# Performance work log

Hardware: AMD Instinct MI355X
Metric: run time of the kernel (lower is better)

Reference implementation:

```python
import jax, jax.numpy as jnp
import numpy as np

B, S, D = 2, 2048, 1024
H = 16
HD = D // H
SCALE = HD ** (-0.5)


def setup_inputs() -> dict:
    key = jax.random.key(0)
    k1, k2, k3, k4 = jax.random.split(key, 4)
    x = jax.random.normal(k1, (B, S, D), dtype=jnp.float32)
    # nn.Linear-style init scale to keep activations sane
    w_qkv = jax.random.normal(k2, (3 * D, D), dtype=jnp.float32) * (D ** -0.5)
    w_out = jax.random.normal(k3, (D, D), dtype=jnp.float32) * (D ** -0.5)
    b_out = jax.random.normal(k4, (D,), dtype=jnp.float32) * 0.01
    return {"x": x, "w_qkv": w_qkv, "w_out": w_out, "b_out": b_out}


def reference(x, w_qkv, w_out, b_out):
    b, s, d = x.shape
    # qkv projection (no bias): [b, s, 3d]
    qkv = jnp.einsum('bsd,ed->bse', x, w_qkv)
    # Rearrange 'b c (e h hd) -> e b h c hd'
    qkv = qkv.reshape(b, s, 3, H, HD).transpose(2, 0, 3, 1, 4)
    # NOTE: original splits as (v, q, k) in that order
    v, q, k = qkv[0], qkv[1], qkv[2]
    # scale applied after matmul, as in the original
    scores = jnp.einsum('bhqd,bhkd->bhqk', q, k) * SCALE
    attn = jax.nn.softmax(scores, axis=-1)
    o = jnp.einsum('bhqk,bhkd->bhqd', attn, v)
    # 'b h c hd -> b c (h hd)'
    o = o.transpose(0, 2, 1, 3).reshape(b, s, d)
    return jnp.einsum('bsd,ed->bse', o, w_out) + b_out
```

## Files before the change

kernel.cpp:

```cpp
#include <hip/hip_runtime.h>
#include <cstdint>
#include <cstddef>

#define BB 2
#define SS 2048
#define DD 1024
#define HH 16
#define HDIM 64

typedef short bf16x8 __attribute__((ext_vector_type(8)));
typedef short bf16x4 __attribute__((ext_vector_type(4)));
typedef float f32x4 __attribute__((ext_vector_type(4)));
typedef float f32x2 __attribute__((ext_vector_type(2)));

union U4S8 { uint4 u; bf16x8 s; };
union U2S4 { uint2 u; bf16x4 s; unsigned short h[4]; };

#if defined(__HIP_DEVICE_COMPILE__)
# if __has_builtin(__builtin_amdgcn_mfma_f32_16x16x16bf16_1k)
#  define MFMA_PV(a, b, c) __builtin_amdgcn_mfma_f32_16x16x16bf16_1k((a), (b), (c), 0, 0, 0)
# else
#  define MFMA_PV(a, b, c) __builtin_amdgcn_mfma_f32_16x16x16_bf16((a), (b), (c), 0, 0, 0)
# endif
# if __has_builtin(__builtin_amdgcn_exp2f)
#  define EXP2(x) __builtin_amdgcn_exp2f(x)
# else
#  define EXP2(x) exp2f(x)
# endif
#else
# define MFMA_PV(a, b, c) (c)
# define EXP2(x) exp2f(x)
#endif

__device__ __forceinline__ unsigned short f2bf(float f) {
    union { float f; unsigned int u; } c; c.f = f;
    unsigned int u = c.u;
    unsigned int r = (u + 0x7FFFu + ((u >> 16) & 1u)) >> 16;
    return (unsigned short)r;
}

__device__ __forceinline__ void async_cp16(const void* g, void* l) {
    __builtin_amdgcn_global_load_lds(
        (const __attribute__((address_space(1))) void*)g,
        (__attribute__((address_space(3))) void*)l, 16, 0, 0);
}

__global__ __launch_bounds__(256) void cvt_all(
    const float* __restrict__ x, const float* __restrict__ wq,
    const float* __restrict__ wo,
    unsigned short* __restrict__ xb, unsigned short* __restrict__ wqb,
    unsigned short* __restrict__ wob) {
    int i = blockIdx.x * 256 + threadIdx.x;
    const float* in; unsigned short* out; int j;
    if (i < 524288)       { in = x;  out = xb;  j = i; }
    else if (i < 917504)  { in = wq; out = wqb; j = i - 524288; }
    else                  { in = wo; out = wob; j = i - 917504; }
    float4 a = ((const float4*)in)[2 * j];
    float4 b = ((const float4*)in)[2 * j + 1];
    union { uint4 u; unsigned short h[8]; } o;
    o.h[0] = f2bf(a.x); o.h[1] = f2bf(a.y); o.h[2] = f2bf(a.z); o.h[3] = f2bf(a.w);
    o.h[4] = f2bf(b.x); o.h[5] = f2bf(b.y); o.h[6] = f2bf(b.z); o.h[7] = f2bf(b.w);
    ((uint4*)out)[j] = o.u;
}

__global__ __launch_bounds__(256) void gemm_qkv(
    const unsigned short* __restrict__ A,
    const unsigned short* __restrict__ Bw,
    unsigned short* __restrict__ qb, unsigned short* __restrict__ kb,
    unsigned short* __restrict__ vb) {
    const int K = 1024;
    __shared__ unsigned short smem[18432];
    int tid = threadIdx.x;
    int lane = tid & 63, wave = tid >> 6;
    int wm = (wave & 1) * 64, wn = (wave >> 1) * 64;
    int m0 = blockIdx.y * 128, n0 = blockIdx.x * 128;
    int lm = lane & 15, lq = lane >> 4;

    f32x4 acc[4][4] = {};

    int sdst = tid * 8;
    const unsigned short* gA = A  + (size_t)(m0 + (tid >> 2)) * K + (tid & 3) * 8;
    const unsigned short* gB = Bw + (size_t)(n0 + (tid >> 2)) * K + (tid & 3) * 8;

#define GSTAGE(k0, buf) do {                                          \
        async_cp16(gA + (k0),          smem + (buf) + sdst);          \
        async_cp16(gA + 64 * K + (k0), smem + (buf) + 2048 + sdst);   \
        async_cp16(gB + (k0),          smem + (buf) + 4096 + sdst);   \
        async_cp16(gB + 64 * K + (k0), smem + (buf) + 6144 + sdst);   \
    } while (0)

    GSTAGE(0, 0);
    for (int k0 = 0; k0 < K; k0 += 64) {
        #pragma unroll
        for (int hf = 0; hf < 2; hf++) {
            int base = hf ? 8192 : 0;
            int obuf = hf ? 0 : 8192;
            __syncthreads();
            int kn = k0 + 32 + hf * 32;
            if (kn < K) GSTAGE(kn, obuf);
            const unsigned short* As = smem + base;
            const unsigned short* Bs = smem + base + 4096;
            U4S8 af[4], bfx[4];
            #pragma unroll
            for (int i = 0; i < 4; i++) {
                af[i].u  = *(const uint4*)(As + (wm + i * 16 + lm) * 32 + lq * 8);
                bfx[i].u = *(const uint4*)(Bs + (wn + i * 16 + lm) * 32 + lq * 8);
            }
            #pragma unroll
            for (int mi = 0; mi < 4; mi++)
                #pragma unroll
                for (int ni = 0; ni < 4; ni++)
                    acc[mi][ni] = __builtin_amdgcn_mfma_f32_16x16x32_bf16(
                        af[mi].s, bfx[ni].s, acc[mi][ni], 0, 0, 0);
        }
    }
#undef GSTAGE
    __syncthreads();

    unsigned short* Lw = smem + wave * 4608;
    int b = m0 >> 11;
    int s_base = (m0 + wm) & 2047;
    if (n0 < 1024) {
        int h = (n0 + wn) >> 6;
        #pragma unroll
        for (int mi = 0; mi < 4; mi++)
            #pragma unroll
            for (int ni = 0; ni < 4; ni++)
                #pragma unroll
                for (int r = 0; r < 4; r++)
                    Lw[(ni * 16 + lm) * 72 + mi * 16 + lq * 4 + r] =
                        f2bf(acc[mi][ni][r]);
        __builtin_amdgcn_wave_barrier();
        unsigned short* vdst = vb + ((size_t)(b * HH + h) * HDIM) * SS + s_base;
        #pragma unroll
        for (int it = 0; it < 8; it++) {
            int hd = it * 8 + (lane >> 3);
            int so = (lane & 7) * 8;
            uint4 val = *(const uint4*)&Lw[hd * 72 + so];
            *(uint4*)(vdst + (size_t)hd * SS + so) = val;
        }
    } else {
        bool isq = n0 < 2048;
        unsigned short* dst = isq ? qb : kb;
        float scale = isq ? 0.18033688f : 1.0f;
        int h = ((n0 + wn) >> 6) & 15;
        #pragma unroll
        for (int mi = 0; mi < 4; mi++)
            #pragma unroll
            for (int ni = 0; ni < 4; ni++)
                #pragma unroll
                for (int r = 0; r < 4; r++)
                    Lw[(mi * 16 + lq * 4 + r) * 72 + ni * 16 + lm] =
                        f2bf(acc[mi][ni][r] * scale);
        __builtin_amdgcn_wave_barrier();
        unsigned short* qdst =
            dst + ((size_t)(b * HH + h) * SS + s_base) * HDIM;
        #pragma unroll
        for (int it = 0; it < 8; it++) {
            int srw = it * 8 + (lane >> 3);
            int so = (lane & 7) * 8;
            uint4 val = *(const uint4*)&Lw[srw * 72 + so];
            *(uint4*)(qdst + (size_t)srw * HDIM + so) = val;
        }
    }
}

__global__ __launch_bounds__(512) void attn(
    const unsigned short* __restrict__ qb,
    const unsigned short* __restrict__ kb,
    const unsigned short* __restrict__ vb,
    unsigned short* __restrict__ ob) {
    int bh = blockIdx.y;
    int q0 = blockIdx.x * 128;
    int tid = threadIdx.x, lane = tid & 63, wave = tid >> 6;
    int grp = wave >> 2;
    int w4  = wave & 3;
    int lm = lane & 15, lq = lane >> 4;

    __shared__ unsigned short smem[32768];
    float* smf = (float*)smem;

    const unsigned short* qg = qb + (size_t)bh * SS * HDIM;
    const unsigned short* kg = kb + (size_t)bh * SS * HDIM;
    const unsigned short* vg = vb + (size_t)bh * HDIM * SS;

    U4S8 qf[2][2];
    #pragma unroll
    for (int qt = 0; qt < 2; qt++)
        #pragma unroll
        for (int ks = 0; ks < 2; ks++)
            qf[qt][ks].u = *(const uint4*)(
                qg + (size_t)(q0 + w4 * 32 + qt * 16 + lm) * HDIM + ks * 32 + lq * 8);

    f32x4 oacc[4][2] = {};
    f32x2 lsum2[2] = {};

    int lm7 = lm & 7;
    int kidx = lm * 64 + 8 * (lq ^ lm7);
    int vidx[4];
    #pragma unroll
    for (int kc = 0; kc < 4; kc++)
        vidx[kc] = lm * 64 + 8 * (((kc << 1) | (lq >> 1)) ^ lm7) + (lq & 1) * 4;

    int srow = tid >> 3;
    int lch  = (tid & 7) ^ (srow & 7);
    int sdst = tid * 8;
    const unsigned short* kpA = kg + (size_t)srow * HDIM + lch * 8;
    const unsigned short* kpB = kpA + 64 * HDIM;
    const unsigned short* vpA = vg + (size_t)srow * SS + lch * 8;
    const unsigned short* vpB = vpA + 64;

    #define STAGE(pbase)                                                       \
        do {                                                                   \
            async_cp16(kpA, smem + (pbase) + sdst);                            \
            async_cp16(kpB, smem + (pbase) + 4096 + sdst);                     \
            async_cp16(vpA, smem + (pbase) + 8192 + sdst);                     \
            async_cp16(vpB, smem + (pbase) + 12288 + sdst);                    \
            kpA += 128 * HDIM; kpB += 128 * HDIM; vpA += 128; vpB += 128;      \
        } while (0)

    STAGE(0);

    for (int kt = 0; kt < SS / 128; kt += 2) {
        #pragma unroll
        for (int hf = 0; hf < 2; hf++) {
            int cbase = hf ? 16384 : 0;
            int obase = hf ? 0 : 16384;
            __syncthreads();
            STAGE(obase);

            int kbase = cbase + grp * 4096;
            int vbase = cbase + 8192 + grp * 4096;

            U2S4 pb[4][2];
            #pragma unroll
            for (int mi = 0; mi < 4; mi++) {
                U4S8 kf0, kf1;
                kf0.u = *(const uint4*)(smem + kbase + mi * 1024 + kidx);
                kf1.u = *(const uint4*)(smem + kbase + mi * 1024 + (kidx ^ 32));
                #pragma unroll
                for (int qt = 0; qt < 2; qt++) {
                    f32x4 sa = {};
                    sa = __builtin_amdgcn_mfma_f32_16x16x32_bf16(kf0.s, qf[qt][0].s, sa, 0, 0, 0);
                    sa = __builtin_amdgcn_mfma_f32_16x16x32_bf16(kf1.s, qf[qt][1].s, sa, 0, 0, 0);
                    float p0 = EXP2(sa[0]);
                    float p1 = EXP2(sa[1]);
                    float p2 = EXP2(sa[2]);
                    float p3 = EXP2(sa[3]);
                    f32x2 a01; a01[0] = p0; a01[1] = p1;
                    f32x2 a23; a23[0] = p2; a23[1] = p3;
                    lsum2[qt] += a01;
                    lsum2[qt] += a23;
                    unsigned int b0 = __float_as_uint(p0) + 0x8000u;
                    unsigned int b1 = __float_as_uint(p1) + 0x8000u;
                    unsigned int b2 = __float_as_uint(p2) + 0x8000u;
                    unsigned int b3 = __float_as_uint(p3) + 0x8000u;
                    pb[mi][qt].u.x = __builtin_amdgcn_perm(b1, b0, 0x07060302u);
                    pb[mi][qt].u.y = __builtin_amdgcn_perm(b3, b2, 0x07060302u);
                }
            }

            #pragma unroll
            for (int mi2 = 0; mi2 < 4; mi2++) {
                #pragma unroll
                for (int kc = 0; kc < 4; kc++) {
                    U2S4 vf;
                    vf.u = *(const uint2*)(smem + vbase + mi2 * 1024 + vidx[kc]);
                    oacc[mi2][0] = MFMA_PV(vf.s, pb[kc][0].s, oacc[mi2][0]);
                    oacc[mi2][1] = MFMA_PV(vf.s, pb[kc][1].s, oacc[mi2][1]);
                }
            }
        }
    }
    #undef STAGE

    float gsum[2];
    #pragma unroll
    for (int qt = 0; qt < 2; qt++) {
        float s = lsum2[qt][0] + lsum2[qt][1];
        s += __shfl_xor(s, 16);
        s += __shfl_xor(s, 32);
        gsum[qt] = s;
    }

    __syncthreads();

    if (grp == 1) {
        float* pub = smf + w4 * 2048;
        #pragma unroll
        for (int mi2 = 0; mi2 < 4; mi2++)
            #pragma unroll
            for (int qt = 0; qt < 2; qt++)
                #pragma unroll
                for (int r = 0; r < 4; r++)
                    pub[(mi2 * 8 + qt * 4 + r) * 64 + lane] = oacc[mi2][qt][r];
        if (lq == 0) {
            smf[8192 + w4 * 32 + lm]      = gsum[0];
            smf[8192 + w4 * 32 + 16 + lm] = gsum[1];
        }
    }
    __syncthreads();

    if (grp == 0) {
        float* pub = smf + w4 * 2048;
        #pragma unroll
        for (int mi2 = 0; mi2 < 4; mi2++)
            #pragma unroll
            for (int qt = 0; qt < 2; qt++)
                #pragma unroll
                for (int r = 0; r < 4; r++)
                    oacc[mi2][qt][r] += pub[(mi2 * 8 + qt * 4 + r) * 64 + lane];
        float inv[2];
        inv[0] = 1.f / (gsum[0] + smf[8192 + w4 * 32 + lm]);
        inv[1] = 1.f / (gsum[1] + smf[8192 + w4 * 32 + 16 + lm]);

        unsigned short* Ow = smem + 17024 + w4 * 2304;
        #pragma unroll
        for (int mi2 = 0; mi2 < 4; mi2++)
            #pragma unroll
            for (int qt = 0; qt < 2; qt++) {
                U2S4 t;
                #pragma unroll
                for (int r = 0; r < 4; r++)
                    t.h[r] = f2bf(oacc[mi2][qt][r] * inv[qt]);
                *(uint2*)&Ow[(qt * 16 + lm) * 72 + mi2 * 16 + lq * 4] = t.u;
            }
        __builtin_amdgcn_wave_barrier();
        int b = bh >> 4, h = bh & 15;
        #pragma unroll
        for (int it = 0; it < 4; it++) {
            int q  = it * 8 + (lane >> 3);
            int off = (lane & 7) * 8;
            uint4 val = *(const uint4*)&Ow[q * 72 + off];
            int srw = q0 + w4 * 32 + q;
            *(uint4*)(ob + (size_t)(b * SS + srw) * DD + h * 64 + off) = val;
        }
    }
}

__global__ __launch_bounds__(256) void gemm_out(
    const unsigned short* __restrict__ A,
    const unsigned short* __restrict__ Bw,
    const float* __restrict__ bias, float* __restrict__ out) {
    const int K = 1024;
    __shared__ unsigned short smem[12288];
    int tid = threadIdx.x;
    int lane = tid & 63, wave = tid >> 6;
    int wm = (wave & 1) * 64, wn = (wave >> 1) * 32;
    int m0 = blockIdx.y * 128, n0 = blockIdx.x * 64;
    int lm = lane & 15, lq = lane >> 4;

    f32x4 acc[4][2] = {};

    int sdst = tid * 8;
    const unsigned short* gA = A  + (size_t)(m0 + (tid >> 2)) * K + (tid & 3) * 8;
    const unsigned short* gB = Bw + (size_t)(n0 + (tid >> 2)) * K + (tid & 3) * 8;

#define OSTAGE(k0, buf) do {                                          \
        async_cp16(gA + (k0),          smem + (buf) + sdst);          \
        async_cp16(gA + 64 * K + (k0), smem + (buf) + 2048 + sdst);   \
        async_cp16(gB + (k0),          smem + (buf) + 4096 + sdst);   \
    } while (0)

    OSTAGE(0, 0);
    for (int k0 = 0; k0 < K; k0 += 64) {
        #pragma unroll
        for (int hf = 0; hf < 2; hf++) {
            int base = hf ? 6144 : 0;
            int obuf = hf ? 0 : 6144;
            __syncthreads();
            int kn = k0 + 32 + hf * 32;
            if (kn < K) OSTAGE(kn, obuf);
            const unsigned short* As = smem + base;
            const unsigned short* Bs = smem + base + 4096;
            U4S8 af[4], bfx[2];
            #pragma unroll
            for (int i = 0; i < 4; i++)
                af[i].u = *(const uint4*)(As + (wm + i * 16 + lm) * 32 + lq * 8);
            #pragma unroll
            for (int i = 0; i < 2; i++)
                bfx[i].u = *(const uint4*)(Bs + (wn + i * 16 + lm) * 32 + lq * 8);
            #pragma unroll
            for (int mi = 0; mi < 4; mi++)
                #pragma unroll
                for (int ni = 0; ni < 2; ni++)
                    acc[mi][ni] = __builtin_amdgcn_mfma_f32_16x16x32_bf16(
                        af[mi].s, bfx[ni].s, acc[mi][ni], 0, 0, 0);
        }
    }
#undef OSTAGE

    #pragma unroll
    for (int mi = 0; mi < 4; mi++) {
        int gr = m0 + wm + mi * 16 + lq * 4;
        #pragma unroll
        for (int ni = 0; ni < 2; ni++) {
            int gc = n0 + wn + ni * 16 + lm;
            float bv = bias[gc];
            #pragma unroll
            for (int r = 0; r < 4; r++)
                out[(size_t)(gr + r) * DD + gc] = acc[mi][ni][r] + bv;
        }
    }
}

extern "C" void kernel_launch(void* const* d_in, const int* in_sizes, int n_in,
                              void* d_out, int out_size, void* d_ws, size_t ws_size,
                              hipStream_t stream) {
    const float* x     = (const float*)d_in[0];
    const float* w_qkv = (const float*)d_in[1];
    const float* w_out = (const float*)d_in[2];
    const float* b_out = (const float*)d_in[3];
    float* out = (float*)d_out;

    unsigned short* ws = (unsigned short*)d_ws;
    const size_t NX = (size_t)BB * SS * DD;
    unsigned short* x_bf    = ws;
    unsigned short* wqkv_bf = x_bf + NX;
    unsigned short* wout_bf = wqkv_bf + 3145728;
    unsigned short* q_buf   = wout_bf + 1048576;
    unsigned short* k_buf   = q_buf + NX;
    unsigned short* v_buf   = k_buf + NX;
    unsigned short* o_buf   = v_buf + NX;

    cvt_all<<<4096, 256, 0, stream>>>(x, w_qkv, w_out, x_bf, wqkv_bf, wout_bf);
    gemm_qkv<<<dim3(24, 32), 256, 0, stream>>>(x_bf, wqkv_bf, q_buf, k_buf, v_buf);
    attn<<<dim3(16, 32), 512, 0, stream>>>(q_buf, k_buf, v_buf, o_buf);
    gemm_out<<<dim3(16, 32), 256, 0, stream>>>(o_buf, wout_bf, b_out, out);
}
```

Baseline: 200.7 us.

## Use 16x16x32 bf16 MFMA for PV product with permuted K row staging

Replaces the four 16x16x16 MFMAs per PV block with two 16x16x32 MFMAs. P fragments are now packed into 8-wide bf16 vectors, and V is read with 16-byte LDS loads. To make the packed P layout line up with the K dimension the wider instruction expects, the K rows are permuted when staged from global memory. This halves the PV MFMA instruction count and the number of V LDS reads, at the cost of a more intricate row index mapping that must stay consistent with the score layout.

```diff
diff --git a/kernel.cpp b/kernel.cpp
--- a/kernel.cpp
+++ b/kernel.cpp
@@ -17,18 +17,12 @@
 union U2S4 { uint2 u; bf16x4 s; unsigned short h[4]; };
 
 #if defined(__HIP_DEVICE_COMPILE__)
-# if __has_builtin(__builtin_amdgcn_mfma_f32_16x16x16bf16_1k)
-#  define MFMA_PV(a, b, c) __builtin_amdgcn_mfma_f32_16x16x16bf16_1k((a), (b), (c), 0, 0, 0)
-# else
-#  define MFMA_PV(a, b, c) __builtin_amdgcn_mfma_f32_16x16x16_bf16((a), (b), (c), 0, 0, 0)
-# endif
 # if __has_builtin(__builtin_amdgcn_exp2f)
 #  define EXP2(x) __builtin_amdgcn_exp2f(x)
 # else
 #  define EXP2(x) exp2f(x)
 # endif
 #else
-# define MFMA_PV(a, b, c) (c)
 # define EXP2(x) exp2f(x)
 #endif
 
@@ -197,17 +191,19 @@
 
     int lm7 = lm & 7;
     int kidx = lm * 64 + 8 * (lq ^ lm7);
-    int vidx[4];
+    int vidx[2];
     #pragma unroll
-    for (int kc = 0; kc < 4; kc++)
-        vidx[kc] = lm * 64 + 8 * (((kc << 1) | (lq >> 1)) ^ lm7) + (lq & 1) * 4;
-
-    int srow = tid >> 3;
-    int lch  = (tid & 7) ^ (srow & 7);
+    for (int kblk = 0; kblk < 2; kblk++)
+        vidx[kblk] = lm * 64 + 8 * (((kblk << 2) | lq) ^ lm7);
+
+    int sr  = tid >> 3;
+    int s5  = sr & 31;
+    int kap = (sr & 32) + (((s5 >> 2) & 3) << 3) + (((s5 >> 4) & 1) << 2) + (s5 & 3);
+    int lch = (tid & 7) ^ (sr & 7);
     int sdst = tid * 8;
-    const unsigned short* kpA = kg + (size_t)srow * HDIM + lch * 8;
+    const unsigned short* kpA = kg + (size_t)kap * HDIM + lch * 8;
     const unsigned short* kpB = kpA + 64 * HDIM;
-    const unsigned short* vpA = vg + (size_t)srow * SS + lch * 8;
+    const unsigned short* vpA = vg + (size_t)sr * SS + lch * 8;
     const unsigned short* vpB = vpA + 64;
 
     #define STAGE(pbase)                                                       \
@@ -232,7 +228,7 @@
             int kbase = cbase + grp * 4096;
             int vbase = cbase + 8192 + grp * 4096;
 
-            U2S4 pb[4][2];
+            U4S8 pb8[2][2];
             #pragma unroll
             for (int mi = 0; mi < 4; mi++) {
                 U4S8 kf0, kf1;
@@ -255,19 +251,23 @@
                     unsigned int b1 = __float_as_uint(p1) + 0x8000u;
                     unsigned int b2 = __float_as_uint(p2) + 0x8000u;
                     unsigned int b3 = __float_as_uint(p3) + 0x8000u;
-                    pb[mi][qt].u.x = __builtin_amdgcn_perm(b1, b0, 0x07060302u);
-                    pb[mi][qt].u.y = __builtin_amdgcn_perm(b3, b2, 0x07060302u);
+                    unsigned int lo = __builtin_amdgcn_perm(b1, b0, 0x07060302u);
+                    unsigned int hi = __builtin_amdgcn_perm(b3, b2, 0x07060302u);
+                    if ((mi & 1) == 0) { pb8[mi >> 1][qt].u.x = lo; pb8[mi >> 1][qt].u.y = hi; }
+                    else               { pb8[mi >> 1][qt].u.z = lo; pb8[mi >> 1][qt].u.w = hi; }
                 }
             }
 
             #pragma unroll
             for (int mi2 = 0; mi2 < 4; mi2++) {
                 #pragma unroll
-                for (int kc = 0; kc < 4; kc++) {
-                    U2S4 vf;
-                    vf.u = *(const uint2*)(smem + vbase + mi2 * 1024 + vidx[kc]);
-                    oacc[mi2][0] = MFMA_PV(vf.s, pb[kc][0].s, oacc[mi2][0]);
-                    oacc[mi2][1] = MFMA_PV(vf.s, pb[kc][1].s, oacc[mi2][1]);
+                for (int kblk = 0; kblk < 2; kblk++) {
+                    U4S8 vf;
+                    vf.u = *(const uint4*)(smem + vbase + mi2 * 1024 + vidx[kblk]);
+                    oacc[mi2][0] = __builtin_amdgcn_mfma_f32_16x16x32_bf16(
+                        vf.s, pb8[kblk][0].s, oacc[mi2][0], 0, 0, 0);
+                    oacc[mi2][1] = __builtin_amdgcn_mfma_f32_16x16x32_bf16(
+                        vf.s, pb8[kblk][1].s, oacc[mi2][1], 0, 0, 0);
                 }
             }
         }
```

New measurement: 194.7 us. 3.0% less time.
